# Performance work log

Measured on AMD Instinct MI355X. Metric: run time of the kernel, lower is better.

## Reference

```python
import jax, jax.numpy as jnp
import numpy as np

N_HEADS = 16
D_MODEL = 1024
HEAD_DIM = D_MODEL // N_HEADS
MASK_FILL = -1e8  # matches torch masked_fill value -100000000.0


def setup_inputs() -> dict:
    key = jax.random.key(0)
    ks = jax.random.split(key, 12)
    B, L, P = 2, 2048, 2048
    s = 1.0 / np.sqrt(D_MODEL).astype(np.float32)
    inp = {
        "q": jax.random.normal(ks[0], (B, L, D_MODEL), dtype=jnp.float32),
        "k": jax.random.normal(ks[1], (B, P, D_MODEL), dtype=jnp.float32),
        "v": jax.random.normal(ks[2], (B, P, D_MODEL), dtype=jnp.float32),
        "attention_mask": jnp.ones((B, P), dtype=bool),
        "Wq": jax.random.normal(ks[3], (D_MODEL, D_MODEL), dtype=jnp.float32) * s,
        "bq": jnp.zeros((D_MODEL,), dtype=jnp.float32),
        "Wk": jax.random.normal(ks[4], (D_MODEL, D_MODEL), dtype=jnp.float32) * s,
        "bk": jnp.zeros((D_MODEL,), dtype=jnp.float32),
        "Wv": jax.random.normal(ks[5], (D_MODEL, D_MODEL), dtype=jnp.float32) * s,
        "bv": jnp.zeros((D_MODEL,), dtype=jnp.float32),
        "Wo": jax.random.normal(ks[6], (D_MODEL, D_MODEL), dtype=jnp.float32) * s,
        "bo": jnp.zeros((D_MODEL,), dtype=jnp.float32),
    }
    return inp


def _split_heads(x):
    # [B, S, D] -> [B, n, S, h]
    B, S, _ = x.shape
    return x.reshape(B, S, N_HEADS, HEAD_DIM).transpose(0, 2, 1, 3)


def reference(q, k, v, attention_mask, Wq, bq, Wk, bk, Wv, bv, Wo, bo):
    # Linear projections (torch Linear: x @ W.T + b)
    qm = _split_heads(q @ Wq.T + bq)
    km = _split_heads(k @ Wk.T + bk)
    vm = _split_heads(v @ Wv.T + bv)
    # scores: [B, n, L, P]
    scores = jnp.einsum('bnlh,bnph->bnlp', qm, km) / np.sqrt(HEAD_DIM).astype(np.float32)
    # mask [B, P] -> [B, 1, 1, P]; fill False positions with -1e8 (as in torch source)
    mask = attention_mask[:, None, None, :]
    scores = jnp.where(mask, scores, MASK_FILL)
    attn = jax.nn.softmax(scores, axis=-1)
    # dropout is identity in eval mode
    out = jnp.einsum('bnlp,bnph->bnlh', attn, vm)
    B, _, L, _ = out.shape
    out = out.transpose(0, 2, 1, 3).reshape(B, L, D_MODEL)
    return out @ Wo.T + bo
```

## Files before the change

### kernel.cpp

```cpp
#include <hip/hip_runtime.h>
#include <hip/hip_bf16.h>

typedef __attribute__((ext_vector_type(8))) __bf16 bf16x8;
typedef __attribute__((ext_vector_type(4))) float f32x4;
typedef __attribute__((ext_vector_type(16))) float f32x16;
typedef __attribute__((ext_vector_type(4))) unsigned short u16x4;
typedef __attribute__((ext_vector_type(2))) unsigned int u32x2;

#define LOG2E 1.4426950408889634f
#define FIXED_MAX 32.0f

__device__ __forceinline__ unsigned short f2bf(float f) {
  union { float f; unsigned int u; } x;
  x.f = f;
  unsigned int u = x.u;
  u += 0x7fffu + ((u >> 16) & 1u);
  return (unsigned short)(u >> 16);
}

__device__ __forceinline__ float fexp2(float x) {
  float r;
  asm("v_exp_f32 %0, %1" : "=v"(r) : "v"(x));
  return r;
}

__device__ __forceinline__ unsigned int cvtpk_bf16(float lo, float hi) {
  unsigned int r;
  asm("v_cvt_pk_bf16_f32 %0, %1, %2" : "=v"(r) : "v"(lo), "v"(hi));
  return r;
}

__device__ __forceinline__ void plswap(unsigned int& a, unsigned int& b) {
  auto r = __builtin_amdgcn_permlane32_swap((int)a, (int)b, false, false);
  a = (unsigned int)r[0];
  b = (unsigned int)r[1];
}

__device__ __forceinline__ void gload_lds16(const void* gsrc, void* lds) {
  __builtin_amdgcn_global_load_lds(
      (const __attribute__((address_space(1))) unsigned int*)gsrc,
      (__attribute__((address_space(3))) unsigned int*)lds, 16, 0, 0);
}

__global__ __launch_bounds__(256) void cvt_all(
    const float* __restrict__ q, const float* __restrict__ k, const float* __restrict__ v,
    const float* __restrict__ w0, const float* __restrict__ w1,
    const float* __restrict__ w2, const float* __restrict__ w3,
    unsigned short* __restrict__ qb, unsigned short* __restrict__ kb,
    unsigned short* __restrict__ vb, unsigned short* __restrict__ w0b,
    unsigned short* __restrict__ w1b, unsigned short* __restrict__ w2b,
    unsigned short* __restrict__ w3b) {
  long idx = (long)blockIdx.x * 256 + threadIdx.x;
  const long QV = 1024L * 1024;
  const long WQ = 256L * 1024;
  const float* src;
  unsigned short* dst;
  long base;
  if (idx < QV)                { src = q;  dst = qb;  base = idx; }
  else if (idx < 2 * QV)       { src = k;  dst = kb;  base = idx - QV; }
  else if (idx < 3 * QV)       { src = v;  dst = vb;  base = idx - 2 * QV; }
  else if (idx < 3 * QV + WQ)  { src = w0; dst = w0b; base = idx - 3 * QV; }
  else if (idx < 3 * QV + 2*WQ){ src = w1; dst = w1b; base = idx - 3 * QV - WQ; }
  else if (idx < 3 * QV + 3*WQ){ src = w2; dst = w2b; base = idx - 3 * QV - 2 * WQ; }
  else                         { src = w3; dst = w3b; base = idx - 3 * QV - 3 * WQ; }
  f32x4 val = *(const f32x4*)(src + base * 4);
  u16x4 o;
#pragma unroll
  for (int i = 0; i < 4; ++i) o[i] = f2bf(val[i]);
  *(u16x4*)(dst + base * 4) = o;
}

template <int MODE>
__global__ __launch_bounds__(256) void gemm_bt(
    const unsigned short* A0, const unsigned short* A1, const unsigned short* A2,
    const unsigned short* W0, const unsigned short* W1, const unsigned short* W2,
    const float* b0, const float* b1, const float* b2,
    void* o0, void* o1, void* o2) {
  __shared__ char smem[32768];
  const int z = blockIdx.z;
  const unsigned short* __restrict__ A = (z == 0) ? A0 : (z == 1) ? A1 : A2;
  const unsigned short* __restrict__ W = (z == 0) ? W0 : (z == 1) ? W1 : W2;
  const float* __restrict__ bias = (z == 0) ? b0 : (z == 1) ? b1 : b2;
  void* __restrict__ out = (z == 0) ? o0 : (z == 1) ? o1 : o2;
  const float oscale = (MODE == 0 && z == 0) ? 0.125f * LOG2E : 1.0f;
  const bool kblocked = (MODE == 0 && z == 1);

  const int tid = threadIdx.x;
  const int lane = tid & 63;
  const int wave = tid >> 6;
  const int wm = (wave >> 1) * 64;
  const int wn = (wave & 1) * 64;
  const int bm0 = blockIdx.x * 128;
  const int bn0 = blockIdx.y * 128;
  const int K = 1024;
  const int srow = tid >> 2;
  const int sg = tid & 3;

  f32x4 acc[4][4] = {};

  auto stageA = [&](int kt, int buf) {
    char* dst = smem + buf * 8192;
#pragma unroll
    for (int h = 0; h < 2; ++h) {
      int row = srow + h * 64;
      int gs = sg ^ ((row >> 1) & 3);
      gload_lds16((const char*)(A + (long)(bm0 + row) * K + kt * 32) + gs * 16,
                  dst + h * 4096 + tid * 16);
    }
  };
  auto stageB = [&](int kt, int buf) {
    char* dst = smem + 16384 + buf * 8192;
#pragma unroll
    for (int h = 0; h < 2; ++h) {
      int row = srow + h * 64;
      int gs = sg ^ ((row >> 1) & 3);
      gload_lds16((const char*)(W + (long)(bn0 + row) * K + kt * 32) + gs * 16,
                  dst + h * 4096 + tid * 16);
    }
  };

  stageA(0, 0);
  stageB(0, 0);
  __syncthreads();

  const int nk = K / 32;
  for (int kt = 0; kt < nk; ++kt) {
    const int cur = kt & 1;
    if (kt + 1 < nk) { stageA(kt + 1, cur ^ 1); stageB(kt + 1, cur ^ 1); }
    char* curA = smem + cur * 8192;
    char* curB = smem + 16384 + cur * 8192;
    const int kb = (lane >> 4) * 16;
    bf16x8 af[4], bfr[4];
#pragma unroll
    for (int i = 0; i < 4; ++i) {
      int row = wm + i * 16 + (lane & 15);
      af[i] = *(const bf16x8*)(curA + row * 64 + (kb ^ (((row >> 1) & 3) << 4)));
    }
#pragma unroll
    for (int j = 0; j < 4; ++j) {
      int row = wn + j * 16 + (lane & 15);
      bfr[j] = *(const bf16x8*)(curB + row * 64 + (kb ^ (((row >> 1) & 3) << 4)));
    }
#pragma unroll
    for (int i = 0; i < 4; ++i)
#pragma unroll
      for (int j = 0; j < 4; ++j)
        acc[i][j] = __builtin_amdgcn_mfma_f32_16x16x32_bf16(af[i], bfr[j], acc[i][j], 0, 0, 0);
    __syncthreads();
  }

#pragma unroll
  for (int i = 0; i < 4; ++i) {
#pragma unroll
    for (int j = 0; j < 4; ++j) {
#pragma unroll
      for (int r = 0; r < 4; ++r) {
        int row = bm0 + wm + i * 16 + (lane >> 4) * 4 + r;
        int col = bn0 + wn + j * 16 + (lane & 15);
        float vv = (acc[i][j][r] + bias[col]) * oscale;
        if (MODE == 0) {
          int bb = row >> 11, ll = row & 2047;
          int hh = col >> 6, hd = col & 63;
          long idx;
          if (kblocked) {
            int pt = ll >> 6, p = ll & 63, g = hd >> 3, e = hd & 7;
            idx = ((((long)((bb * 16 + hh) * 32 + pt)) * 8 + g) * 64 + p) * 8 + e;
          } else {
            idx = (((long)(bb * 16 + hh) * 2048 + ll) << 6) + hd;
          }
          ((unsigned short*)out)[idx] = f2bf(vv);
        } else {
          ((float*)out)[(long)row * 1024 + col] = vv;
        }
      }
    }
  }
}

__global__ __launch_bounds__(256) void transpose_v(const unsigned short* __restrict__ Vm,
                                                   unsigned short* __restrict__ Vt) {
  __shared__ unsigned short t[64][68];
  const int bh = blockIdx.y;
  const int pt = blockIdx.x;
  const int p0 = pt * 64;
  const int tid = threadIdx.x;
#pragma unroll
  for (int it = 0; it < 4; ++it) {
    int idx = it * 256 + tid;
    int r = idx >> 4;
    int c4 = (idx & 15) * 4;
    *(u16x4*)&t[r][c4] = *(const u16x4*)(Vm + ((long)bh * 2048 + p0 + r) * 64 + c4);
  }
  __syncthreads();
#pragma unroll
  for (int it = 0; it < 4; ++it) {
    int idx = it * 256 + tid;
    int hd = idx >> 4;
    int pp4 = (idx & 15) * 4;
    int g = pp4 >> 3, e0 = pp4 & 7;
    u16x4 v;
#pragma unroll
    for (int j = 0; j < 4; ++j) v[j] = t[pp4 + j][hd];
    *(u16x4*)(Vt + ((((long)(bh * 32 + pt)) * 8 + g) * 64 + hd) * 8 + e0) = v;
  }
}

__global__ __launch_bounds__(256, 4) void attn_fwd(
    const unsigned short* __restrict__ Qm,
    const unsigned short* __restrict__ Kblk,
    const unsigned short* __restrict__ Vblk,
    const int* __restrict__ mask,
    unsigned short* __restrict__ ao) {
  __shared__ char smem[37504];
  char* const Kl = smem;
  char* const Vl = smem + 16384;
  unsigned short* const maskb = (unsigned short*)(smem + 32768);
  float* const lsums = (float*)(smem + 36864);
  int* const allm = (int*)(smem + 37376);

  const int tid = threadIdx.x, lane = tid & 63, wave = tid >> 6;
  const int kv = wave & 1;
  const int qg = wave >> 1;
  const int h2 = lane >> 5;
  const int ql = lane & 31;
  const int bh = blockIdx.y, b = bh >> 4, hh = bh & 15;
  const int q0 = blockIdx.x * 64;
  const unsigned short* Qbase = Qm + ((long)bh * 2048 + q0 + qg * 32) * 64;
  const char* Kg = (const char*)(Kblk + (long)bh * 2048 * 64);
  const char* Vg = (const char*)(Vblk + (long)bh * 2048 * 64);

  auto stage_pair = [&](int s) {
#pragma unroll
    for (int c = 0; c < 4; ++c) {
      int off = (c * 256 + tid) * 16;
      gload_lds16(Kg + (long)s * 16384 + off, Kl + off);
      gload_lds16(Vg + (long)s * 16384 + off, Vl + off);
    }
  };

  stage_pair(0);

  {
    const int* mrow = mask + b * 2048;
    int p8 = tid * 8;
    int ok = 1;
#pragma unroll
    for (int i = 0; i < 4; ++i) {
      int m0 = mrow[p8 + 2 * i];
      int m1 = mrow[p8 + 2 * i + 1];
      ok &= (m0 != 0) & (m1 != 0);
      unsigned int lo = m0 ? 0u : 1u;
      unsigned int hi = m1 ? 0u : 1u;
      *(unsigned int*)(maskb + p8 + 2 * i) = lo | (hi << 16);
    }
    unsigned long long bal = __ballot(ok != 0);
    if (lane < 8) allm[wave * 8 + lane] = (int)(((bal >> (lane * 8)) & 0xFFull) == 0xFFull);
  }

  bf16x8 qf[4];
#pragma unroll
  for (int ks = 0; ks < 4; ++ks)
    qf[ks] = *(const bf16x8*)(Qbase + (long)ql * 64 + ks * 16 + h2 * 8);

  f32x16 o0 = {}, o1 = {};
  float lsum = 0.f;
  const char* const Kc = Kl + kv * 8192;
  const char* const Vc = Vl + kv * 8192;
  __syncthreads();

  for (int s = 0; s < 16; ++s) {
    const int pt = 2 * s + kv;

    f32x16 s0 = {}, s1 = {};
#pragma unroll
    for (int ks = 0; ks < 4; ++ks) {
      int gl = ks * 2 + h2;
      bf16x8 k0 = *(const bf16x8*)(Kc + gl * 1024 + ql * 16);
      bf16x8 k1 = *(const bf16x8*)(Kc + gl * 1024 + 512 + ql * 16);
      s0 = __builtin_amdgcn_mfma_f32_32x32x16_bf16(k0, qf[ks], s0, 0, 0, 0);
      s1 = __builtin_amdgcn_mfma_f32_32x32x16_bf16(k1, qf[ks], s1, 0, 0, 0);
    }

    if (!allm[pt]) {
#pragma unroll
      for (int rq = 0; rq < 4; ++rq) {
        u16x4 m0 = *(const u16x4*)(maskb + pt * 64 + rq * 8 + 4 * h2);
        u16x4 m1 = *(const u16x4*)(maskb + pt * 64 + 32 + rq * 8 + 4 * h2);
#pragma unroll
        for (int i = 0; i < 4; ++i) {
          s0[rq * 4 + i] = m0[i] ? -1.0e8f : s0[rq * 4 + i];
          s1[rq * 4 + i] = m1[i] ? -1.0e8f : s1[rq * 4 + i];
        }
      }
    }

#pragma unroll
    for (int i = 0; i < 16; ++i) {
      float p = fexp2(s0[i] - FIXED_MAX);
      s0[i] = p; lsum += p;
    }
#pragma unroll
    for (int i = 0; i < 16; ++i) {
      float p = fexp2(s1[i] - FIXED_MAX);
      s1[i] = p; lsum += p;
    }

    bf16x8 pa[4];
    {
      union { unsigned int w[4]; bf16x8 v; } u;
      unsigned int w0, w1, w2, w3;
      w0 = cvtpk_bf16(s0[0],  s0[1]);  w1 = cvtpk_bf16(s0[2],  s0[3]);
      w2 = cvtpk_bf16(s0[4],  s0[5]);  w3 = cvtpk_bf16(s0[6],  s0[7]);
      plswap(w0, w2); plswap(w1, w3);
      u.w[0] = w0; u.w[1] = w1; u.w[2] = w2; u.w[3] = w3; pa[0] = u.v;
      w0 = cvtpk_bf16(s0[8],  s0[9]);  w1 = cvtpk_bf16(s0[10], s0[11]);
      w2 = cvtpk_bf16(s0[12], s0[13]); w3 = cvtpk_bf16(s0[14], s0[15]);
      plswap(w0, w2); plswap(w1, w3);
      u.w[0] = w0; u.w[1] = w1; u.w[2] = w2; u.w[3] = w3; pa[1] = u.v;
      w0 = cvtpk_bf16(s1[0],  s1[1]);  w1 = cvtpk_bf16(s1[2],  s1[3]);
      w2 = cvtpk_bf16(s1[4],  s1[5]);  w3 = cvtpk_bf16(s1[6],  s1[7]);
      plswap(w0, w2); plswap(w1, w3);
      u.w[0] = w0; u.w[1] = w1; u.w[2] = w2; u.w[3] = w3; pa[2] = u.v;
      w0 = cvtpk_bf16(s1[8],  s1[9]);  w1 = cvtpk_bf16(s1[10], s1[11]);
      w2 = cvtpk_bf16(s1[12], s1[13]); w3 = cvtpk_bf16(s1[14], s1[15]);
      plswap(w0, w2); plswap(w1, w3);
      u.w[0] = w0; u.w[1] = w1; u.w[2] = w2; u.w[3] = w3; pa[3] = u.v;
    }

#pragma unroll
    for (int kb = 0; kb < 4; ++kb) {
      int gl = kb * 2 + h2;
      bf16x8 v0 = *(const bf16x8*)(Vc + gl * 1024 + ql * 16);
      bf16x8 v1 = *(const bf16x8*)(Vc + gl * 1024 + 512 + ql * 16);
      o0 = __builtin_amdgcn_mfma_f32_32x32x16_bf16(v0, pa[kb], o0, 0, 0, 0);
      o1 = __builtin_amdgcn_mfma_f32_32x32x16_bf16(v1, pa[kb], o1, 0, 0, 0);
    }

    __syncthreads();
    if (s + 1 < 16) {
      stage_pair(s + 1);
      __syncthreads();
    }
  }

  float lf = lsum + __shfl_xor(lsum, 32);
  if (kv == 1) {
    char* Oc = smem + qg * 16384;
#pragma unroll
    for (int rq = 0; rq < 4; ++rq) {
      f32x4 w0 = {o0[rq*4+0], o0[rq*4+1], o0[rq*4+2], o0[rq*4+3]};
      int d4 = (rq * 8 + 4 * h2) * 4;
      *(f32x4*)(Oc + ql * 256 + (d4 ^ ((ql & 7) << 5))) = w0;
      f32x4 w1 = {o1[rq*4+0], o1[rq*4+1], o1[rq*4+2], o1[rq*4+3]};
      int d41 = 128 + d4;
      *(f32x4*)(Oc + ql * 256 + (d41 ^ ((ql & 7) << 5))) = w1;
    }
    if (h2 == 0) lsums[qg * 64 + ql] = lf;
  }
  __syncthreads();
  if (kv == 0) {
    const char* Oc = smem + qg * 16384;
#pragma unroll
    for (int rq = 0; rq < 4; ++rq) {
      int d4 = (rq * 8 + 4 * h2) * 4;
      f32x4 w0 = *(const f32x4*)(Oc + ql * 256 + (d4 ^ ((ql & 7) << 5)));
      f32x4 w1 = *(const f32x4*)(Oc + ql * 256 + ((128 + d4) ^ ((ql & 7) << 5)));
#pragma unroll
      for (int i = 0; i < 4; ++i) { o0[rq*4+i] += w0[i]; o1[rq*4+i] += w1[i]; }
    }
    lf += lsums[qg * 64 + ql];
    float inv = 1.0f / lf;
    unsigned short* aop = ao + ((long)(b * 2048 + q0 + qg * 32 + ql) << 10) + hh * 64;
#pragma unroll
    for (int rq = 0; rq < 4; ++rq) {
      unsigned int lo = cvtpk_bf16(o0[rq * 4 + 0] * inv, o0[rq * 4 + 1] * inv);
      unsigned int hi = cvtpk_bf16(o0[rq * 4 + 2] * inv, o0[rq * 4 + 3] * inv);
      u32x2 st = {lo, hi};
      *(u32x2*)(aop + rq * 8 + 4 * h2) = st;
    }
#pragma unroll
    for (int rq = 0; rq < 4; ++rq) {
      unsigned int lo = cvtpk_bf16(o1[rq * 4 + 0] * inv, o1[rq * 4 + 1] * inv);
      unsigned int hi = cvtpk_bf16(o1[rq * 4 + 2] * inv, o1[rq * 4 + 3] * inv);
      u32x2 st = {lo, hi};
      *(u32x2*)(aop + 32 + rq * 8 + 4 * h2) = st;
    }
  }
}

extern "C" void kernel_launch(void* const* d_in, const int* in_sizes, int n_in,
                              void* d_out, int out_size, void* d_ws, size_t ws_size,
                              hipStream_t stream) {
  const float* q = (const float*)d_in[0];
  const float* k = (const float*)d_in[1];
  const float* v = (const float*)d_in[2];
  const int* mask = (const int*)d_in[3];
  const float* Wq = (const float*)d_in[4];
  const float* bq = (const float*)d_in[5];
  const float* Wk = (const float*)d_in[6];
  const float* bk = (const float*)d_in[7];
  const float* Wv = (const float*)d_in[8];
  const float* bv = (const float*)d_in[9];
  const float* Wo = (const float*)d_in[10];
  const float* bo = (const float*)d_in[11];

  char* ws = (char*)d_ws;
  unsigned short* qb  = (unsigned short*)(ws + (0L << 20));
  unsigned short* kb  = (unsigned short*)(ws + (8L << 20));
  unsigned short* vb  = (unsigned short*)(ws + (16L << 20));
  unsigned short* wqb = (unsigned short*)(ws + (24L << 20));
  unsigned short* wkb = (unsigned short*)(ws + (26L << 20));
  unsigned short* wvb = (unsigned short*)(ws + (28L << 20));
  unsigned short* wob = (unsigned short*)(ws + (30L << 20));
  unsigned short* Qh  = (unsigned short*)(ws + (32L << 20));
  unsigned short* Kb  = (unsigned short*)(ws + (40L << 20));
  unsigned short* Vh  = (unsigned short*)(ws + (48L << 20));
  unsigned short* Vb  = (unsigned short*)(ws + (56L << 20));
  unsigned short* aob = (unsigned short*)(ws + (64L << 20));

  cvt_all<<<16384, 256, 0, stream>>>(q, k, v, Wq, Wk, Wv, Wo,
                                     qb, kb, vb, wqb, wkb, wvb, wob);
  gemm_bt<0><<<dim3(32, 8, 3), 256, 0, stream>>>(qb, kb, vb, wqb, wkb, wvb,
                                                 bq, bk, bv, Qh, Kb, Vh);
  transpose_v<<<dim3(32, 32), 256, 0, stream>>>(Vh, Vb);
  attn_fwd<<<dim3(32, 32), 256, 0, stream>>>(Qh, Kb, Vb, mask, aob);
  gemm_bt<1><<<dim3(32, 8, 1), 256, 0, stream>>>(aob, aob, aob, wob, wob, wob,
                                                 bo, bo, bo, d_out, d_out, d_out);
  (void)in_sizes; (void)n_in; (void)out_size; (void)ws_size;
}
```

Baseline: 136.7 us.

## Double-buffer K/V tiles in attention and shrink output GEMM tile to 64 rows

The attention kernel now keeps two K/V LDS buffers and issues the next tile's loads before computing on the current one. This removes the extra barrier and load stall per iteration, at the cost of roughly doubling LDS per block, which may reduce occupancy from the 4 blocks requested. Separately, the output-projection GEMM uses 64-row tiles with each wave covering 32 columns, doubling the grid to 512 blocks so the 256 CUs are better filled.

Result: no change. 135.5 us (-0.9%).

```diff
diff --git a/kernel.cpp b/kernel.cpp
--- a/kernel.cpp
+++ b/kernel.cpp
@@ -77,6 +77,8 @@
     const float* b0, const float* b1, const float* b2,
     void* o0, void* o1, void* o2) {
   __shared__ char smem[32768];
+  constexpr int BM = (MODE == 1) ? 64 : 128;
+  constexpr int NF = (MODE == 1) ? 2 : 4;
   const int z = blockIdx.z;
   const unsigned short* __restrict__ A = (z == 0) ? A0 : (z == 1) ? A1 : A2;
   const unsigned short* __restrict__ W = (z == 0) ? W0 : (z == 1) ? W1 : W2;
@@ -88,20 +90,20 @@
   const int tid = threadIdx.x;
   const int lane = tid & 63;
   const int wave = tid >> 6;
-  const int wm = (wave >> 1) * 64;
-  const int wn = (wave & 1) * 64;
-  const int bm0 = blockIdx.x * 128;
+  const int wm = (MODE == 1) ? 0 : (wave >> 1) * 64;
+  const int wn = (MODE == 1) ? wave * 32 : (wave & 1) * 64;
+  const int bm0 = blockIdx.x * BM;
   const int bn0 = blockIdx.y * 128;
   const int K = 1024;
   const int srow = tid >> 2;
   const int sg = tid & 3;
 
-  f32x4 acc[4][4] = {};
+  f32x4 acc[4][NF] = {};
 
   auto stageA = [&](int kt, int buf) {
     char* dst = smem + buf * 8192;
 #pragma unroll
-    for (int h = 0; h < 2; ++h) {
+    for (int h = 0; h < BM / 64; ++h) {
       int row = srow + h * 64;
       int gs = sg ^ ((row >> 1) & 3);
       gload_lds16((const char*)(A + (long)(bm0 + row) * K + kt * 32) + gs * 16,
@@ -130,21 +132,21 @@
     char* curA = smem + cur * 8192;
     char* curB = smem + 16384 + cur * 8192;
     const int kb = (lane >> 4) * 16;
-    bf16x8 af[4], bfr[4];
+    bf16x8 af[4], bfr[NF];
 #pragma unroll
     for (int i = 0; i < 4; ++i) {
       int row = wm + i * 16 + (lane & 15);
       af[i] = *(const bf16x8*)(curA + row * 64 + (kb ^ (((row >> 1) & 3) << 4)));
     }
 #pragma unroll
-    for (int j = 0; j < 4; ++j) {
+    for (int j = 0; j < NF; ++j) {
       int row = wn + j * 16 + (lane & 15);
       bfr[j] = *(const bf16x8*)(curB + row * 64 + (kb ^ (((row >> 1) & 3) << 4)));
     }
 #pragma unroll
     for (int i = 0; i < 4; ++i)
 #pragma unroll
-      for (int j = 0; j < 4; ++j)
+      for (int j = 0; j < NF; ++j)
         acc[i][j] = __builtin_amdgcn_mfma_f32_16x16x32_bf16(af[i], bfr[j], acc[i][j], 0, 0, 0);
     __syncthreads();
   }
@@ -152,7 +154,7 @@
 #pragma unroll
   for (int i = 0; i < 4; ++i) {
 #pragma unroll
-    for (int j = 0; j < 4; ++j) {
+    for (int j = 0; j < NF; ++j) {
 #pragma unroll
       for (int r = 0; r < 4; ++r) {
         int row = bm0 + wm + i * 16 + (lane >> 4) * 4 + r;
@@ -211,12 +213,12 @@
     const unsigned short* __restrict__ Vblk,
     const int* __restrict__ mask,
     unsigned short* __restrict__ ao) {
-  __shared__ char smem[37504];
+  __shared__ char smem[70272];
   char* const Kl = smem;
-  char* const Vl = smem + 16384;
-  unsigned short* const maskb = (unsigned short*)(smem + 32768);
-  float* const lsums = (float*)(smem + 36864);
-  int* const allm = (int*)(smem + 37376);
+  char* const Vl = smem + 32768;
+  unsigned short* const maskb = (unsigned short*)(smem + 65536);
+  float* const lsums = (float*)(smem + 69632);
+  int* const allm = (int*)(smem + 70144);
 
   const int tid = threadIdx.x, lane = tid & 63, wave = tid >> 6;
   const int kv = wave & 1;
@@ -229,16 +231,20 @@
   const char* Kg = (const char*)(Kblk + (long)bh * 2048 * 64);
   const char* Vg = (const char*)(Vblk + (long)bh * 2048 * 64);
 
-  auto stage_pair = [&](int s) {
+  auto stage_pair = [&](int s, int buf) {
+    char* dk = Kl + buf * 16384;
+    char* dv = Vl + buf * 16384;
+    const char* sk = Kg + (long)s * 16384;
+    const char* sv = Vg + (long)s * 16384;
 #pragma unroll
     for (int c = 0; c < 4; ++c) {
       int off = (c * 256 + tid) * 16;
-      gload_lds16(Kg + (long)s * 16384 + off, Kl + off);
-      gload_lds16(Vg + (long)s * 16384 + off, Vl + off);
+      gload_lds16(sk + off, dk + off);
+      gload_lds16(sv + off, dv + off);
     }
   };
 
-  stage_pair(0);
+  stage_pair(0, 0);
 
   {
     const int* mrow = mask + b * 2048;
@@ -264,12 +270,14 @@
 
   f32x16 o0 = {}, o1 = {};
   float lsum = 0.f;
-  const char* const Kc = Kl + kv * 8192;
-  const char* const Vc = Vl + kv * 8192;
   __syncthreads();
 
   for (int s = 0; s < 16; ++s) {
+    const int cur = s & 1;
+    if (s + 1 < 16) stage_pair(s + 1, cur ^ 1);
     const int pt = 2 * s + kv;
+    const char* Kc = Kl + cur * 16384 + kv * 8192;
+    const char* Vc = Vl + cur * 16384 + kv * 8192;
 
     f32x16 s0 = {}, s1 = {};
 #pragma unroll
@@ -337,10 +345,6 @@
     }
 
     __syncthreads();
-    if (s + 1 < 16) {
-      stage_pair(s + 1);
-      __syncthreads();
-    }
   }
 
   float lf = lsum + __shfl_xor(lsum, 32);
@@ -424,7 +428,7 @@
                                                  bq, bk, bv, Qh, Kb, Vh);
   transpose_v<<<dim3(32, 32), 256, 0, stream>>>(Vh, Vb);
   attn_fwd<<<dim3(32, 32), 256, 0, stream>>>(Qh, Kb, Vb, mask, aob);
-  gemm_bt<1><<<dim3(32, 8, 1), 256, 0, stream>>>(aob, aob, aob, wob, wob, wob,
+  gemm_bt<1><<<dim3(64, 8, 1), 256, 0, stream>>>(aob, aob, aob, wob, wob, wob,
                                                  bo, bo, bo, d_out, d_out, d_out);
   (void)in_sizes; (void)n_in; (void)out_size; (void)ws_size;
 }
```
